# Performance work log

Hardware: AMD Instinct MI355X
Metric: run time of the kernel (lower is better)

The kernel has to match this reference:

```python
import jax, jax.numpy as jnp
import numpy as np
from jax import lax

VOCAB, NUM_CLASSES = 21128, 53
EMB, FILT, K = 128, 128, 3
B, L = 512, 512


def setup_inputs() -> dict:
    key = jax.random.key(0)
    ks = jax.random.split(key, 8)
    char_ids = jax.random.randint(ks[0], (B, L), 0, VOCAB, dtype=jnp.int64 if jax.config.jax_enable_x64 else jnp.int32)
    pos_e1 = jax.random.randint(ks[1], (B,), 0, L - 1, dtype=jnp.int32)
    pos_e2 = jax.random.randint(ks[2], (B,), 0, L - 1, dtype=jnp.int32)
    emb_table = jax.random.normal(ks[3], (VOCAB, EMB), dtype=jnp.float32) * 0.02
    emb_table = emb_table.at[0].set(0.0)  # padding_idx=0
    conv_w = jax.random.normal(ks[4], (FILT, EMB, K), dtype=jnp.float32) * (1.0 / np.sqrt(EMB * K))
    conv_b = jax.random.normal(ks[5], (FILT,), dtype=jnp.float32) * 0.01
    fc_w = jax.random.normal(ks[6], (NUM_CLASSES, FILT * 3), dtype=jnp.float32) * (1.0 / np.sqrt(FILT * 3))
    fc_b = jax.random.normal(ks[7], (NUM_CLASSES,), dtype=jnp.float32) * 0.01
    return {"char_ids": char_ids, "pos_e1": pos_e1, "pos_e2": pos_e2,
            "emb_table": emb_table, "conv_w": conv_w, "conv_b": conv_b,
            "fc_w": fc_w, "fc_b": fc_b}


def reference(char_ids, pos_e1, pos_e2, emb_table, conv_w, conv_b, fc_w, fc_b):
    b, seq = char_ids.shape
    x = emb_table[char_ids]                      # (b, L, E)
    x = jnp.transpose(x, (0, 2, 1))              # (b, E, L)
    conv_out = lax.conv_general_dilated(
        x, conv_w, window_strides=(1,), padding=[(K // 2, K // 2)],
        dimension_numbers=("NCH", "OIH", "NCH"))
    conv_out = jax.nn.relu(conv_out + conv_b[None, :, None])  # (b, F, L)

    # sort + clip entity boundaries, replicate e1==e2 -> e2=e1+1 adjustment
    e1 = jnp.clip(jnp.minimum(pos_e1, pos_e2), 0, seq)
    e2 = jnp.clip(jnp.maximum(pos_e1, pos_e2), 0, seq)
    e2 = jnp.where(e1 == e2, jnp.minimum(e1 + 1, seq), e2)

    idx = jnp.arange(seq)[None, :]               # (1, L)
    m1 = idx < jnp.maximum(e1, 1)[:, None]       # [:e1] or [:1] if e1==0
    m2 = (idx >= e1[:, None]) & (idx < e2[:, None])
    m3 = idx >= jnp.minimum(e2, seq - 1)[:, None]  # [e2:] or last col if e2==L

    neg = jnp.float32(-jnp.inf)
    def seg_max(mask):
        return jnp.max(jnp.where(mask[:, None, :], conv_out, neg), axis=-1)  # (b, F)

    pooled = jnp.concatenate([seg_max(m1), seg_max(m2), seg_max(m3)], axis=-1)  # (b, 3F)
    return pooled @ fc_w.T + fc_b
```

## Files before the change

### kernel.cpp

```cpp
#include <hip/hip_runtime.h>
#include <stdint.h>

#define VOCAB 21128
#define NUMC  53
#define EMB   128
#define SEQ   512
#define BATCH 512

typedef __bf16 bf16x8 __attribute__((ext_vector_type(8)));
typedef float f32x4 __attribute__((ext_vector_type(4)));
typedef __attribute__((address_space(3))) void lds_void;
typedef const __attribute__((address_space(1))) void glob_void;

__device__ __forceinline__ unsigned int f2bf1(float f) {
    union { float f; unsigned int u; } v; v.f = f;
    return (v.u + 0x7FFFu + ((v.u >> 16) & 1u)) >> 16;
}
__device__ __forceinline__ unsigned int pack2(float a, float b) {
    return f2bf1(a) | (f2bf1(b) << 16);
}

__global__ void prep_kernel(const float* __restrict__ emb, const float* __restrict__ cw,
                            unsigned short* __restrict__ Tb, unsigned short* __restrict__ Wp) {
    int idx = blockIdx.x * blockDim.x + threadIdx.x;
    const int n8 = VOCAB * EMB / 8;
    if (idx < n8) {
        const float4* src = (const float4*)emb + (size_t)idx * 2;
        float4 a = src[0], b = src[1];
        uint4 o;
        o.x = pack2(a.x, a.y);
        o.y = pack2(a.z, a.w);
        o.z = pack2(b.x, b.y);
        o.w = pack2(b.z, b.w);
        *(uint4*)(Tb + (size_t)idx * 8) = o;
    }
    if (idx < 12 * 8 * 64 * 8) {
        int j = idx & 7, l = (idx >> 3) & 63, g = (idx >> 9) & 7, s = idx >> 12;
        int kk = s * 32 + (l >> 4) * 8 + j;
        int f = g * 16 + (l & 15);
        int tap = kk >> 7, e = kk & 127;
        Wp[idx] = (unsigned short)f2bf1(cw[(f * EMB + e) * 3 + tap]);
    }
}

__launch_bounds__(512)
__global__ void pcnn_tile(const int* __restrict__ cid, const int* __restrict__ p1,
                          const int* __restrict__ p2,
                          const unsigned short* __restrict__ Tb,
                          const unsigned short* __restrict__ Wp,
                          float* __restrict__ Pd) {
    __shared__ __align__(16) unsigned short xs[130 * 128];
    __shared__ float pstage[2][3][128];

    const int bx   = blockIdx.x;
    const int b    = bx >> 2;
    const int tq   = bx & 3;
    const int tid  = threadIdx.x;
    const int lane = tid & 63;
    const int w    = tid >> 6;
    const int wm   = w & 1;
    const int wn   = w >> 1;
    const int quad = lane >> 4;
    const int lc   = lane & 15;

    const int* crow = cid + (size_t)b * SEQ;
    const char* TbB = (const char*)Tb;
    char* xsB = (char*)xs;

#pragma unroll
    for (int i = 0; i < 5; ++i) {
        int task = tid + 512 * i;
        if (task < 2080) {
            int r = task >> 4, c = task & 15;
            int p = tq * 128 + r - 1;
            unsigned int id = (p >= 0 && p < SEQ) ? (unsigned int)crow[p] : 0u;
            int cs = c ^ (r & 15);
            __builtin_amdgcn_global_load_lds(
                (glob_void*)(TbB + (size_t)id * 256u + cs * 16),
                (lds_void*)(xsB + task * 16), 16, 0, 0);
        }
    }

    int e1 = min(p1[b], p2[b]);
    int e2 = max(p1[b], p2[b]);
    if (e1 == e2) e2 = min(e1 + 1, SEQ);
    const int e1m = max(e1, 1);

    __syncthreads();

    f32x4 acc[4][2];
#pragma unroll
    for (int mt = 0; mt < 4; ++mt)
#pragma unroll
        for (int nt = 0; nt < 2; ++nt)
            acc[mt][nt] = (f32x4){0.f, 0.f, 0.f, 0.f};

#pragma unroll
    for (int s = 0; s < 12; ++s) {
        const int tap = s >> 2;
        const int q   = (s & 3) * 4 + quad;
        const int cs  = q ^ ((lc + tap) & 15);
        bf16x8 b0 = *(const bf16x8*)(Wp + (size_t)((s * 8 + wn * 2) * 64 + lane) * 8);
        bf16x8 b1 = *(const bf16x8*)(Wp + (size_t)((s * 8 + wn * 2 + 1) * 64 + lane) * 8);
        bf16x8 af[4];
#pragma unroll
        for (int mt = 0; mt < 4; ++mt) {
            int r = wm * 64 + mt * 16 + lc + tap;
            af[mt] = *(const bf16x8*)(xs + r * 128 + cs * 8);
        }
#pragma unroll
        for (int mt = 0; mt < 4; ++mt) {
            acc[mt][0] = __builtin_amdgcn_mfma_f32_16x16x32_bf16(af[mt], b0, acc[mt][0], 0, 0, 0);
            acc[mt][1] = __builtin_amdgcn_mfma_f32_16x16x32_bf16(af[mt], b1, acc[mt][1], 0, 0, 0);
        }
    }

    float smax[3][2];
#pragma unroll
    for (int s3 = 0; s3 < 3; ++s3) { smax[s3][0] = -1e30f; smax[s3][1] = -1e30f; }

#pragma unroll
    for (int mt = 0; mt < 4; ++mt)
#pragma unroll
        for (int reg = 0; reg < 4; ++reg) {
            int p = tq * 128 + wm * 64 + mt * 16 + quad * 4 + reg;
            float a0 = (p < e1m) ? 0.f : -2e30f;
            float a1 = (p >= e1 && p < e2) ? 0.f : -2e30f;
            float a2 = (p >= e2) ? 0.f : -2e30f;
#pragma unroll
            for (int nt = 0; nt < 2; ++nt) {
                float v = acc[mt][nt][reg];
                smax[0][nt] = fmaxf(smax[0][nt], v + a0);
                smax[1][nt] = fmaxf(smax[1][nt], v + a1);
                smax[2][nt] = fmaxf(smax[2][nt], v + a2);
            }
        }

#pragma unroll
    for (int s3 = 0; s3 < 3; ++s3)
#pragma unroll
        for (int nt = 0; nt < 2; ++nt) {
            float v = smax[s3][nt];
            v = fmaxf(v, __shfl_xor(v, 16));
            v = fmaxf(v, __shfl_xor(v, 32));
            smax[s3][nt] = v;
        }
    if (lane < 16) {
#pragma unroll
        for (int s3 = 0; s3 < 3; ++s3)
#pragma unroll
            for (int nt = 0; nt < 2; ++nt)
                pstage[wm][s3][(wn * 2 + nt) * 16 + lc] = smax[s3][nt];
    }
    __syncthreads();

    if (tid < 384) {
        int s3 = tid >> 7, f = tid & 127;
        Pd[((size_t)b * 4 + tq) * 384 + tid] = fmaxf(pstage[0][s3][f], pstage[1][s3][f]);
    }
}

__launch_bounds__(256)
__global__ void pcnn_combine(const float* __restrict__ Pd, const float* __restrict__ cb,
                             const float* __restrict__ fcw, const float* __restrict__ fcb,
                             float* __restrict__ out) {
    __shared__ float pooled[384];
    __shared__ float fcred[NUMC][4];
    const int b = blockIdx.x;
    const int tid = threadIdx.x;

    for (int j = tid; j < 384; j += 256) {
        const float* pp = Pd + (size_t)b * 4 * 384 + j;
        float m = fmaxf(fmaxf(pp[0], pp[384]), fmaxf(pp[768], pp[1152]));
        pooled[j] = fmaxf(m + cb[j & 127], 0.f);
    }
    __syncthreads();

    if (tid < 212) {
        int c = tid >> 2, q = tid & 3;
        const float* wrow = fcw + (size_t)c * 384 + q * 96;
        const float* pp   = pooled + q * 96;
        float sum = 0.f;
#pragma unroll 8
        for (int i = 0; i < 96; ++i) sum += wrow[i] * pp[i];
        fcred[c][q] = sum;
    }
    __syncthreads();
    if (tid < NUMC)
        out[(size_t)b * NUMC + tid] =
            fcred[tid][0] + fcred[tid][1] + fcred[tid][2] + fcred[tid][3] + fcb[tid];
}

extern "C" void kernel_launch(void* const* d_in, const int* in_sizes, int n_in,
                              void* d_out, int out_size, void* d_ws, size_t ws_size,
                              hipStream_t stream) {
    const int*   cid = (const int*)d_in[0];
    const int*   p1  = (const int*)d_in[1];
    const int*   p2  = (const int*)d_in[2];
    const float* emb = (const float*)d_in[3];
    const float* cw  = (const float*)d_in[4];
    const float* cb  = (const float*)d_in[5];
    const float* fcw = (const float*)d_in[6];
    const float* fcb = (const float*)d_in[7];
    float* out = (float*)d_out;

    unsigned short* Tb = (unsigned short*)d_ws;
    unsigned short* Wp = (unsigned short*)((char*)d_ws + (size_t)VOCAB * EMB * 2);
    float*          Pd = (float*)((char*)d_ws + (size_t)VOCAB * EMB * 2 + 98304);

    const int n8 = VOCAB * EMB / 8;
    const int prep_threads = 256;
    const int prep_blocks  = (n8 + prep_threads - 1) / prep_threads;
    prep_kernel<<<prep_blocks, prep_threads, 0, stream>>>(emb, cw, Tb, Wp);
    pcnn_tile<<<BATCH * 4, 512, 0, stream>>>(cid, p1, p2, Tb, Wp, Pd);
    pcnn_combine<<<BATCH, 256, 0, stream>>>(Pd, cb, fcw, fcb, out);
}
```

Baseline: 114.3 us.

## Fuse combine kernel into tile kernel via last-block atomic ticket

Removes the separate combine launch. Each tile block increments a per-batch atomic counter after writing its partial maxima, and the block that draws the last ticket does the cross-tile max, bias, ReLU and the FC projection. The counters are zeroed in the prep kernel. This saves a kernel launch and its gap, at the cost of extra LDS, a fence and atomic per block, and a tail of serial FC work in the last block of each batch row.

```diff
diff --git a/kernel.cpp b/kernel.cpp
--- a/kernel.cpp
+++ b/kernel.cpp
@@ -21,7 +21,8 @@
 }
 
 __global__ void prep_kernel(const float* __restrict__ emb, const float* __restrict__ cw,
-                            unsigned short* __restrict__ Tb, unsigned short* __restrict__ Wp) {
+                            unsigned short* __restrict__ Tb, unsigned short* __restrict__ Wp,
+                            int* __restrict__ cnt) {
     int idx = blockIdx.x * blockDim.x + threadIdx.x;
     const int n8 = VOCAB * EMB / 8;
     if (idx < n8) {
@@ -41,6 +42,7 @@
         int tap = kk >> 7, e = kk & 127;
         Wp[idx] = (unsigned short)f2bf1(cw[(f * EMB + e) * 3 + tap]);
     }
+    if (idx < BATCH) cnt[idx] = 0;
 }
 
 __launch_bounds__(512)
@@ -48,9 +50,17 @@
                           const int* __restrict__ p2,
                           const unsigned short* __restrict__ Tb,
                           const unsigned short* __restrict__ Wp,
-                          float* __restrict__ Pd) {
+                          const float* __restrict__ cb,
+                          const float* __restrict__ fcw,
+                          const float* __restrict__ fcb,
+                          float* __restrict__ Pd,
+                          float* __restrict__ out,
+                          int* __restrict__ cnt) {
     __shared__ __align__(16) unsigned short xs[130 * 128];
     __shared__ float pstage[2][3][128];
+    __shared__ float pooled[384];
+    __shared__ float fcred[NUMC][4];
+    __shared__ int ticket;
 
     const int bx   = blockIdx.x;
     const int b    = bx >> 2;
@@ -158,37 +168,38 @@
         int s3 = tid >> 7, f = tid & 127;
         Pd[((size_t)b * 4 + tq) * 384 + tid] = fmaxf(pstage[0][s3][f], pstage[1][s3][f]);
     }
-}
-
-__launch_bounds__(256)
-__global__ void pcnn_combine(const float* __restrict__ Pd, const float* __restrict__ cb,
-                             const float* __restrict__ fcw, const float* __restrict__ fcb,
-                             float* __restrict__ out) {
-    __shared__ float pooled[384];
-    __shared__ float fcred[NUMC][4];
-    const int b = blockIdx.x;
-    const int tid = threadIdx.x;
-
-    for (int j = tid; j < 384; j += 256) {
-        const float* pp = Pd + (size_t)b * 4 * 384 + j;
-        float m = fmaxf(fmaxf(pp[0], pp[384]), fmaxf(pp[768], pp[1152]));
-        pooled[j] = fmaxf(m + cb[j & 127], 0.f);
-    }
-    __syncthreads();
-
-    if (tid < 212) {
-        int c = tid >> 2, q = tid & 3;
-        const float* wrow = fcw + (size_t)c * 384 + q * 96;
-        const float* pp   = pooled + q * 96;
-        float sum = 0.f;
+    __syncthreads();
+
+    if (tid == 0) {
+        __threadfence();
+        ticket = atomicAdd(&cnt[b], 1);
+    }
+    __syncthreads();
+
+    if (ticket == 3) {
+        __threadfence();
+
+        if (tid < 384) {
+            const float* pp = Pd + (size_t)b * 4 * 384 + tid;
+            float m = fmaxf(fmaxf(pp[0], pp[384]), fmaxf(pp[768], pp[1152]));
+            pooled[tid] = fmaxf(m + cb[tid & 127], 0.f);
+        }
+        __syncthreads();
+
+        if (tid < 212) {
+            int c = tid >> 2, q = tid & 3;
+            const float* wrow = fcw + (size_t)c * 384 + q * 96;
+            const float* pp   = pooled + q * 96;
+            float sum = 0.f;
 #pragma unroll 8
-        for (int i = 0; i < 96; ++i) sum += wrow[i] * pp[i];
-        fcred[c][q] = sum;
-    }
-    __syncthreads();
-    if (tid < NUMC)
-        out[(size_t)b * NUMC + tid] =
-            fcred[tid][0] + fcred[tid][1] + fcred[tid][2] + fcred[tid][3] + fcb[tid];
+            for (int i = 0; i < 96; ++i) sum += wrow[i] * pp[i];
+            fcred[c][q] = sum;
+        }
+        __syncthreads();
+        if (tid < NUMC)
+            out[(size_t)b * NUMC + tid] =
+                fcred[tid][0] + fcred[tid][1] + fcred[tid][2] + fcred[tid][3] + fcb[tid];
+    }
 }
 
 extern "C" void kernel_launch(void* const* d_in, const int* in_sizes, int n_in,
@@ -207,11 +218,11 @@
     unsigned short* Tb = (unsigned short*)d_ws;
     unsigned short* Wp = (unsigned short*)((char*)d_ws + (size_t)VOCAB * EMB * 2);
     float*          Pd = (float*)((char*)d_ws + (size_t)VOCAB * EMB * 2 + 98304);
+    int*            cnt = (int*)((char*)d_ws + (size_t)VOCAB * EMB * 2 + 98304 + 3145728);
 
     const int n8 = VOCAB * EMB / 8;
     const int prep_threads = 256;
     const int prep_blocks  = (n8 + prep_threads - 1) / prep_threads;
-    prep_kernel<<<prep_blocks, prep_threads, 0, stream>>>(emb, cw, Tb, Wp);
-    pcnn_tile<<<BATCH * 4, 512, 0, stream>>>(cid, p1, p2, Tb, Wp, Pd);
-    pcnn_combine<<<BATCH, 256, 0, stream>>>(Pd, cb, fcw, fcb, out);
-}
+    prep_kernel<<<prep_blocks, prep_threads, 0, stream>>>(emb, cw, Tb, Wp, cnt);
+    pcnn_tile<<<BATCH * 4, 512, 0, stream>>>(cid, p1, p2, Tb, Wp, cb, fcw, fcb, Pd, out, cnt);
+}
```

Result: slower. 417.8 us (+265.5%).

## Precompute per-vocab conv projections and gather-sum them instead of per-sequence GEMM

Applied to the files above, without the earlier changes.

Because the convolution is linear in the embeddings, the kernel first multiplies the whole vocabulary table by all three conv taps into a bf16 projection table P, then each sequence tile just gathers and sums three projected rows per position before segment max-pooling. This replaces the per-sequence MFMA GEMM over all batch positions with a much smaller vocab-sized GEMM plus a memory-bound gather. It adds a large intermediate table and an extra bf16 rounding of the projected values, and moves the cost to scattered reads of P.

```diff
diff --git a/kernel.cpp b/kernel.cpp
--- a/kernel.cpp
+++ b/kernel.cpp
@@ -9,8 +9,6 @@
 
 typedef __bf16 bf16x8 __attribute__((ext_vector_type(8)));
 typedef float f32x4 __attribute__((ext_vector_type(4)));
-typedef __attribute__((address_space(3))) void lds_void;
-typedef const __attribute__((address_space(1))) void glob_void;
 
 __device__ __forceinline__ unsigned int f2bf1(float f) {
     union { float f; unsigned int u; } v; v.f = f;
@@ -18,6 +16,9 @@
 }
 __device__ __forceinline__ unsigned int pack2(float a, float b) {
     return f2bf1(a) | (f2bf1(b) << 16);
+}
+__device__ __forceinline__ float b2f(unsigned short u) {
+    union { float f; unsigned int i; } v; v.i = ((unsigned int)u) << 16; return v.f;
 }
 
 __global__ void prep_kernel(const float* __restrict__ emb, const float* __restrict__ cw,
@@ -43,42 +44,76 @@
     }
 }
 
-__launch_bounds__(512)
-__global__ void pcnn_tile(const int* __restrict__ cid, const int* __restrict__ p1,
-                          const int* __restrict__ p2,
-                          const unsigned short* __restrict__ Tb,
-                          const unsigned short* __restrict__ Wp,
-                          float* __restrict__ Pd) {
-    __shared__ __align__(16) unsigned short xs[130 * 128];
-    __shared__ float pstage[2][3][128];
-
-    const int bx   = blockIdx.x;
-    const int b    = bx >> 2;
-    const int tq   = bx & 3;
+__launch_bounds__(256)
+__global__ void pcnn_vgemm(const unsigned short* __restrict__ Tb,
+                           const unsigned short* __restrict__ Wp,
+                           unsigned short* __restrict__ P) {
     const int tid  = threadIdx.x;
     const int lane = tid & 63;
-    const int w    = tid >> 6;
-    const int wm   = w & 1;
-    const int wn   = w >> 1;
+    const int wn   = tid >> 6;
     const int quad = lane >> 4;
     const int lc   = lane & 15;
+    const int row0 = blockIdx.x * 64;
+
+    f32x4 acc[3][4][2];
+#pragma unroll
+    for (int t = 0; t < 3; ++t)
+#pragma unroll
+        for (int mt = 0; mt < 4; ++mt)
+#pragma unroll
+            for (int nt = 0; nt < 2; ++nt)
+                acc[t][mt][nt] = (f32x4){0.f, 0.f, 0.f, 0.f};
+
+#pragma unroll
+    for (int s = 0; s < 12; ++s) {
+        const int tap = s >> 2;
+        const int q   = (s & 3) * 4 + quad;
+        bf16x8 b0 = *(const bf16x8*)(Wp + (size_t)((s * 8 + wn * 2) * 64 + lane) * 8);
+        bf16x8 b1 = *(const bf16x8*)(Wp + (size_t)((s * 8 + wn * 2 + 1) * 64 + lane) * 8);
+#pragma unroll
+        for (int mt = 0; mt < 4; ++mt) {
+            bf16x8 a = *(const bf16x8*)(Tb + (size_t)(row0 + mt * 16 + lc) * 128 + q * 8);
+            acc[tap][mt][0] = __builtin_amdgcn_mfma_f32_16x16x32_bf16(a, b0, acc[tap][mt][0], 0, 0, 0);
+            acc[tap][mt][1] = __builtin_amdgcn_mfma_f32_16x16x32_bf16(a, b1, acc[tap][mt][1], 0, 0, 0);
+        }
+    }
+
+#pragma unroll
+    for (int tap = 0; tap < 3; ++tap)
+#pragma unroll
+        for (int mt = 0; mt < 4; ++mt) {
+            int grb = row0 + mt * 16 + quad * 4;
+#pragma unroll
+            for (int nt = 0; nt < 2; ++nt) {
+                int col = tap * 128 + (wn * 2 + nt) * 16 + lc;
+#pragma unroll
+                for (int reg = 0; reg < 4; ++reg) {
+                    int gr = grb + reg;
+                    if (gr < VOCAB)
+                        P[(size_t)gr * 384 + col] = (unsigned short)f2bf1(acc[tap][mt][nt][reg]);
+                }
+            }
+        }
+}
+
+__launch_bounds__(256)
+__global__ void pcnn_gather(const int* __restrict__ cid, const int* __restrict__ p1,
+                            const int* __restrict__ p2,
+                            const unsigned short* __restrict__ P,
+                            float* __restrict__ Pd) {
+    __shared__ int idsB[130];
+    __shared__ float pstage[2][3][128];
+
+    const int bx  = blockIdx.x;
+    const int b   = bx >> 2;
+    const int tq  = bx & 3;
+    const int tid = threadIdx.x;
 
     const int* crow = cid + (size_t)b * SEQ;
-    const char* TbB = (const char*)Tb;
-    char* xsB = (char*)xs;
-
-#pragma unroll
-    for (int i = 0; i < 5; ++i) {
-        int task = tid + 512 * i;
-        if (task < 2080) {
-            int r = task >> 4, c = task & 15;
-            int p = tq * 128 + r - 1;
-            unsigned int id = (p >= 0 && p < SEQ) ? (unsigned int)crow[p] : 0u;
-            int cs = c ^ (r & 15);
-            __builtin_amdgcn_global_load_lds(
-                (glob_void*)(TbB + (size_t)id * 256u + cs * 16),
-                (lds_void*)(xsB + task * 16), 16, 0, 0);
-        }
+    if (tid < 130) {
+        int p = tq * 128 + tid - 1;
+        unsigned int id = (p >= 0 && p < SEQ) ? (unsigned int)crow[p] : 0u;
+        idsB[tid] = (int)(id * 768u);
     }
 
     int e1 = min(p1[b], p2[b]);
@@ -88,75 +123,35 @@
 
     __syncthreads();
 
-    f32x4 acc[4][2];
-#pragma unroll
-    for (int mt = 0; mt < 4; ++mt)
-#pragma unroll
-        for (int nt = 0; nt < 2; ++nt)
-            acc[mt][nt] = (f32x4){0.f, 0.f, 0.f, 0.f};
-
-#pragma unroll
-    for (int s = 0; s < 12; ++s) {
-        const int tap = s >> 2;
-        const int q   = (s & 3) * 4 + quad;
-        const int cs  = q ^ ((lc + tap) & 15);
-        bf16x8 b0 = *(const bf16x8*)(Wp + (size_t)((s * 8 + wn * 2) * 64 + lane) * 8);
-        bf16x8 b1 = *(const bf16x8*)(Wp + (size_t)((s * 8 + wn * 2 + 1) * 64 + lane) * 8);
-        bf16x8 af[4];
-#pragma unroll
-        for (int mt = 0; mt < 4; ++mt) {
-            int r = wm * 64 + mt * 16 + lc + tap;
-            af[mt] = *(const bf16x8*)(xs + r * 128 + cs * 8);
-        }
-#pragma unroll
-        for (int mt = 0; mt < 4; ++mt) {
-            acc[mt][0] = __builtin_amdgcn_mfma_f32_16x16x32_bf16(af[mt], b0, acc[mt][0], 0, 0, 0);
-            acc[mt][1] = __builtin_amdgcn_mfma_f32_16x16x32_bf16(af[mt], b1, acc[mt][1], 0, 0, 0);
-        }
-    }
-
-    float smax[3][2];
-#pragma unroll
-    for (int s3 = 0; s3 < 3; ++s3) { smax[s3][0] = -1e30f; smax[s3][1] = -1e30f; }
-
-#pragma unroll
-    for (int mt = 0; mt < 4; ++mt)
-#pragma unroll
-        for (int reg = 0; reg < 4; ++reg) {
-            int p = tq * 128 + wm * 64 + mt * 16 + quad * 4 + reg;
-            float a0 = (p < e1m) ? 0.f : -2e30f;
-            float a1 = (p >= e1 && p < e2) ? 0.f : -2e30f;
-            float a2 = (p >= e2) ? 0.f : -2e30f;
-#pragma unroll
-            for (int nt = 0; nt < 2; ++nt) {
-                float v = acc[mt][nt][reg];
-                smax[0][nt] = fmaxf(smax[0][nt], v + a0);
-                smax[1][nt] = fmaxf(smax[1][nt], v + a1);
-                smax[2][nt] = fmaxf(smax[2][nt], v + a2);
-            }
-        }
-
-#pragma unroll
-    for (int s3 = 0; s3 < 3; ++s3)
-#pragma unroll
-        for (int nt = 0; nt < 2; ++nt) {
-            float v = smax[s3][nt];
-            v = fmaxf(v, __shfl_xor(v, 16));
-            v = fmaxf(v, __shfl_xor(v, 32));
-            smax[s3][nt] = v;
-        }
-    if (lane < 16) {
-#pragma unroll
-        for (int s3 = 0; s3 < 3; ++s3)
-#pragma unroll
-            for (int nt = 0; nt < 2; ++nt)
-                pstage[wm][s3][(wn * 2 + nt) * 16 + lc] = smax[s3][nt];
-    }
-    __syncthreads();
-
-    if (tid < 384) {
-        int s3 = tid >> 7, f = tid & 127;
-        Pd[((size_t)b * 4 + tq) * 384 + tid] = fmaxf(pstage[0][s3][f], pstage[1][s3][f]);
+    const int f    = tid & 127;
+    const int half = tid >> 7;
+    const char* Pb = (const char*)P;
+    const int o0 = f * 2;
+    const int o1 = 256 + f * 2;
+    const int o2 = 512 + f * 2;
+
+    float smax0 = -1e30f, smax1 = -1e30f, smax2 = -1e30f;
+
+#pragma unroll 4
+    for (int pass = 0; pass < 64; ++pass) {
+        int ll = pass * 2 + half;
+        int p  = tq * 128 + ll;
+        float v = b2f(*(const unsigned short*)(Pb + idsB[ll]     + o0))
+                + b2f(*(const unsigned short*)(Pb + idsB[ll + 1] + o1))
+                + b2f(*(const unsigned short*)(Pb + idsB[ll + 2] + o2));
+        smax0 = fmaxf(smax0, v + ((p < e1m)           ? 0.f : -2e30f));
+        smax1 = fmaxf(smax1, v + ((p >= e1 && p < e2) ? 0.f : -2e30f));
+        smax2 = fmaxf(smax2, v + ((p >= e2)           ? 0.f : -2e30f));
+    }
+
+    pstage[half][0][f] = smax0;
+    pstage[half][1][f] = smax1;
+    pstage[half][2][f] = smax2;
+    __syncthreads();
+
+    for (int j = tid; j < 384; j += 256) {
+        int s3 = j >> 7, ff = j & 127;
+        Pd[((size_t)b * 4 + tq) * 384 + j] = fmaxf(pstage[0][s3][ff], pstage[1][s3][ff]);
     }
 }
 
@@ -206,12 +201,16 @@
 
     unsigned short* Tb = (unsigned short*)d_ws;
     unsigned short* Wp = (unsigned short*)((char*)d_ws + (size_t)VOCAB * EMB * 2);
-    float*          Pd = (float*)((char*)d_ws + (size_t)VOCAB * EMB * 2 + 98304);
+    unsigned short* P  = (unsigned short*)((char*)d_ws + (size_t)VOCAB * EMB * 2 + 98304);
+    float*          Pd = (float*)((char*)d_ws + (size_t)VOCAB * EMB * 2 + 98304
+                                  + (size_t)VOCAB * 384 * 2);
 
     const int n8 = VOCAB * EMB / 8;
     const int prep_threads = 256;
     const int prep_blocks  = (n8 + prep_threads - 1) / prep_threads;
+    const int gemm_blocks  = (VOCAB + 63) / 64;
     prep_kernel<<<prep_blocks, prep_threads, 0, stream>>>(emb, cw, Tb, Wp);
-    pcnn_tile<<<BATCH * 4, 512, 0, stream>>>(cid, p1, p2, Tb, Wp, Pd);
+    pcnn_vgemm<<<gemm_blocks, 256, 0, stream>>>(Tb, Wp, P);
+    pcnn_gather<<<BATCH * 4, 256, 0, stream>>>(cid, p1, p2, P, Pd);
     pcnn_combine<<<BATCH, 256, 0, stream>>>(Pd, cb, fcw, fcb, out);
 }
```

Result: slower. 122.9 us (+7.5%).
